# Optimization experiments

Hardware: AMD Instinct MI355X
Metric: run time of the kernel (lower is better)

The kernel has to match this reference:

```python
import jax, jax.numpy as jnp
import numpy as np

B, T, F = 1024, 512, 8        # batch, in_seq_len, n_in_feat
E, H, O, TO = 16, 32, 1, 24   # emb_size, hid_size, output_size, out_seq_len


def setup_inputs() -> dict:
    key = jax.random.key(0)
    ks = jax.random.split(key, 24)
    def n(k, shape, scale=0.1):
        return (jax.random.normal(k, shape, jnp.float32) * scale)
    return dict(
        x=jax.random.normal(ks[0], (B, T, F), jnp.float32),
        y=jax.random.normal(ks[1], (B, TO, O), jnp.float32),
        enc_emb_w=n(ks[2], (E, F)), enc_emb_b=n(ks[3], (E,)),
        enc_wih_f=n(ks[4], (3 * H, E)), enc_whh_f=n(ks[5], (3 * H, H)),
        enc_bih_f=n(ks[6], (3 * H,)), enc_bhh_f=n(ks[7], (3 * H,)),
        enc_wih_b=n(ks[8], (3 * H, E)), enc_whh_b=n(ks[9], (3 * H, H)),
        enc_bih_b=n(ks[10], (3 * H,)), enc_bhh_b=n(ks[11], (3 * H,)),
        enc_act_w=n(ks[12], (H, 2 * H)), enc_act_b=n(ks[13], (H,)),
        attn_w=n(ks[14], (H, 3 * H)),   # Linear(2H + H -> H), input order (s, enc_out)
        attn_v=n(ks[15], (1, H)),
        dec_emb_w=n(ks[16], (E, O)), dec_emb_b=n(ks[17], (E,)),
        dec_wih=n(ks[18], (3 * H, 2 * H + E)), dec_whh=n(ks[19], (3 * H, H)),
        dec_bih=n(ks[20], (3 * H,)), dec_bhh=n(ks[21], (3 * H,)),
        fc_w=n(ks[22], (O, 3 * H + E)), fc_b=n(ks[23], (O,)),
    )


def gru_cell(x_t, h, wih, whh, bih, bhh):
    # PyTorch GRU cell: gate order (r, z, n)
    gi = x_t @ wih.T + bih
    gh = h @ whh.T + bhh
    ir, iz, inn = jnp.split(gi, 3, axis=-1)
    hr, hz, hn = jnp.split(gh, 3, axis=-1)
    r = jax.nn.sigmoid(ir + hr)
    z = jax.nn.sigmoid(iz + hz)
    cand = jnp.tanh(inn + r * hn)
    return (1.0 - z) * cand + z * h


def reference(x, y, enc_emb_w, enc_emb_b, enc_wih_f, enc_whh_f, enc_bih_f, enc_bhh_f,
              enc_wih_b, enc_whh_b, enc_bih_b, enc_bhh_b, enc_act_w, enc_act_b,
              attn_w, attn_v, dec_emb_w, dec_emb_b, dec_wih, dec_whh, dec_bih, dec_bhh,
              fc_w, fc_b):
    # ----- Encoder (dropout=identity, eval mode; teacher_forcing_ratio=0 -> deterministic) -----
    xt = x.transpose(1, 0, 2)                                  # (T,B,F)
    emb = jax.nn.relu(xt @ enc_emb_w.T + enc_emb_b)            # (T,B,E)
    h0 = jnp.zeros((x.shape[0], H), x.dtype)

    def mkstep(wih, whh, bih, bhh):
        def step(h, xt_):
            hn = gru_cell(xt_, h, wih, whh, bih, bhh)
            return hn, hn
        return step

    hTf, outf = jax.lax.scan(mkstep(enc_wih_f, enc_whh_f, enc_bih_f, enc_bhh_f), h0, emb)
    hTb, outb = jax.lax.scan(mkstep(enc_wih_b, enc_whh_b, enc_bih_b, enc_bhh_b), h0, emb[::-1])
    outb = outb[::-1]
    enc_out = jnp.concatenate([outf, outb], axis=-1)            # (T,B,2H)
    s0 = jnp.tanh(jnp.concatenate([hTf, hTb], axis=-1) @ enc_act_w.T + enc_act_b)  # (B,H)

    Ws, We = attn_w[:, :H], attn_w[:, H:]                       # split concat(s, enc_out)
    enc_proj = enc_out @ We.T                                   # (T,B,H), step-invariant
    enc_out_btd = enc_out.transpose(1, 0, 2)                    # (B,T,2H)

    dec_in0 = x[:, -1, 0:1]                                     # (B,1)

    def dec_step(carry, _):
        dec_in, s = carry
        e = jnp.tanh(s @ Ws.T + enc_proj)                       # (T,B,H)
        scores = (e @ attn_v.T)[..., 0]                         # (T,B)
        # NOTE: faithful to original: torch.softmax(a, dim=1) normalizes over BATCH axis
        a = jax.nn.softmax(scores, axis=1).T                    # (B,T)
        ctx = jnp.einsum('bt,btd->bd', a, enc_out_btd)          # (B,2H)
        embd = jax.nn.relu(dec_in @ dec_emb_w.T + dec_emb_b)    # (B,E)
        rnn_in = jnp.concatenate([embd, ctx], axis=-1)          # (B,E+2H)
        s_new = gru_cell(rnn_in, s, dec_wih, dec_whh, dec_bih, dec_bhh)
        cat = jnp.concatenate([s_new, ctx, embd], axis=-1)      # (B,H+2H+E)
        pred = cat @ fc_w.T + fc_b                              # (B,O)
        return (pred, s_new), pred

    _, preds = jax.lax.scan(dec_step, (dec_in0, s0), None, length=TO)  # (TO,B,O)
    return preds.transpose(1, 0, 2)                             # (B,TO,O)
```

## Files before the change

kernel.cpp:

```cpp
#include <hip/hip_runtime.h>
#include <hip/hip_bf16.h>
#include <stdint.h>
#include <stddef.h>


#define LOG2E 1.44269504088896340736f

__device__ __forceinline__ float fast_sigmoid(float x){
    return __builtin_amdgcn_rcpf(1.f + __builtin_amdgcn_exp2f(-LOG2E * x));
}
__device__ __forceinline__ float fast_tanh(float x){
    return 1.f - 2.f * __builtin_amdgcn_rcpf(1.f + __builtin_amdgcn_exp2f(2.f * LOG2E * x));
}
__device__ __forceinline__ float bflo(unsigned u){ return __uint_as_float(u << 16); }
__device__ __forceinline__ float bfhi(unsigned u){ return __uint_as_float(u & 0xffff0000u); }
__device__ __forceinline__ float bperm(int addr, float v){
    return __int_as_float(__builtin_amdgcn_ds_bpermute(addr, __float_as_int(v)));
}

__global__ __launch_bounds__(256, 2) void enc_kernel(
    const float* __restrict__ x,
    const float* __restrict__ emb_w, const float* __restrict__ emb_b,
    const float* __restrict__ wih_f, const float* __restrict__ whh_f,
    const float* __restrict__ bih_f, const float* __restrict__ bhh_f,
    const float* __restrict__ wih_b, const float* __restrict__ whh_b,
    const float* __restrict__ bih_b, const float* __restrict__ bhh_b,
    __hip_bfloat16* __restrict__ enc_outT, float* __restrict__ hT)
{
    int tid = threadIdx.x;
    int l = tid & 63;
    int wv = tid >> 6;
    int j = l & 31;
    int p = l >> 5;
    int S = blockIdx.x * 4 + wv;
    int dir = S >> 10;
    int b = S & 1023;
    const float* wih = dir ? wih_b : wih_f;
    const float* whh = dir ? whh_b : whh_f;
    const float* bih = dir ? bih_b : bih_f;
    const float* bhh = dir ? bhh_b : bhh_f;

    float wr[8], wz[8], wn[8];
#pragma unroll
    for (int e = 0; e < 8; e++){
        int ee = 8 * p + e;
        wr[e] = wih[j * 16 + ee];
        wz[e] = wih[(32 + j) * 16 + ee];
        wn[e] = wih[(64 + j) * 16 + ee];
    }
    float ur[16], uz[16], un[16];
#pragma unroll
    for (int k = 0; k < 16; k++){
        int kk = 16 * p + k;
        ur[k] = whh[j * 32 + kk];
        uz[k] = whh[(32 + j) * 32 + kk];
        un[k] = whh[(64 + j) * 32 + kk];
    }
    float c_r  = p ? 0.f : (bih[j] + bhh[j]);
    float c_z  = p ? 0.f : (bih[32 + j] + bhh[32 + j]);
    float c_ni = p ? 0.f : bih[64 + j];
    float c_nh = p ? 0.f : bhh[64 + j];

    float ew[8];
#pragma unroll
    for (int f = 0; f < 8; f++) ew[f] = emb_w[(l & 15) * 8 + f];
    float ebias = emb_b[l & 15];

    int aE[8], aH[16];
#pragma unroll
    for (int i = 0; i < 8; i++) aE[i] = 4 * (8 * p + i);
#pragma unroll
    for (int i = 0; i < 16; i++) aH[i] = 4 * (16 * p + i);
    int aX = 4 * (l ^ 32);

    float h = 0.f;
    const float* xp = x + (size_t)b * 4096 + (dir ? 511 * 8 : 0);
    __hip_bfloat16* op = enc_outT + ((size_t)b * 512 + (dir ? 511 : 0)) * 64 + dir * 32 + j;
    int xstep = dir ? -8 : 8;
    ptrdiff_t ostep = dir ? -64 : 64;

    float4 cx0 = ((const float4*)xp)[0];
    float4 cx1 = ((const float4*)xp)[1];

    for (int it = 0; it < 512; ++it){
        const float* np = (it == 511) ? xp : (xp + xstep);
        float4 nx0 = ((const float4*)np)[0];
        float4 nx1 = ((const float4*)np)[1];

        float e0 = ebias;
        e0 = fmaf(cx0.x, ew[0], e0); e0 = fmaf(cx0.y, ew[1], e0);
        e0 = fmaf(cx0.z, ew[2], e0); e0 = fmaf(cx0.w, ew[3], e0);
        e0 = fmaf(cx1.x, ew[4], e0); e0 = fmaf(cx1.y, ew[5], e0);
        e0 = fmaf(cx1.z, ew[6], e0); e0 = fmaf(cx1.w, ew[7], e0);
        float me = fmaxf(e0, 0.f);

        float Ar = c_r, Az = c_z, Ani = c_ni, Anh = c_nh;
#pragma unroll
        for (int i = 0; i < 8; i++){
            float ev = bperm(aE[i], me);
            Ar = fmaf(ev, wr[i], Ar);
            Az = fmaf(ev, wz[i], Az);
            Ani = fmaf(ev, wn[i], Ani);
        }
#pragma unroll
        for (int i = 0; i < 16; i++){
            float hk = bperm(aH[i], h);
            Ar = fmaf(hk, ur[i], Ar);
            Az = fmaf(hk, uz[i], Az);
            Anh = fmaf(hk, un[i], Anh);
        }
        Ar  += bperm(aX, Ar);
        Az  += bperm(aX, Az);
        Ani += bperm(aX, Ani);
        Anh += bperm(aX, Anh);

        float r = fast_sigmoid(Ar);
        float z = fast_sigmoid(Az);
        float cand = fast_tanh(fmaf(r, Anh, Ani));
        h = (1.f - z) * cand + z * h;

        *op = __float2bfloat16(h);
        cx0 = nx0; cx1 = nx1;
        xp = np; op += ostep;
    }
    hT[b * 64 + dir * 32 + j] = h;
}

__global__ __launch_bounds__(256) void s0_kernel(
    const float* __restrict__ hT, const float* __restrict__ act_w, const float* __restrict__ act_b,
    const float* __restrict__ attn_w, const float* __restrict__ x,
    float* __restrict__ s, float* __restrict__ sWs, float* __restrict__ dec_in,
    float* __restrict__ denom)
{
    if (blockIdx.x == 0){
        for (int i = threadIdx.x; i < 24 * 512; i += 256) denom[i] = 0.f;
    }
    int j = threadIdx.x & 31, g = threadIdx.x >> 5;
    int b = blockIdx.x * 8 + g;
    float acc = act_b[j];
    const float4* aw = (const float4*)(act_w + j * 64);
    const float4* hp = (const float4*)(hT + b * 64);
#pragma unroll
    for (int c = 0; c < 16; c++){
        float4 wv = aw[c]; float4 hv = hp[c];
        acc = fmaf(hv.x, wv.x, acc); acc = fmaf(hv.y, wv.y, acc);
        acc = fmaf(hv.z, wv.z, acc); acc = fmaf(hv.w, wv.w, acc);
    }
    float s0v = fast_tanh(acc);
    s[b * 32 + j] = s0v;
    __shared__ float ssh[8][33];
    ssh[g][j] = s0v;
    __syncthreads();
    float a = 0.f;
    const float4* wsp = (const float4*)(attn_w + j * 96);
#pragma unroll
    for (int c = 0; c < 8; c++){
        float4 wv = wsp[c];
        a = fmaf(ssh[g][4 * c + 0], wv.x, a);
        a = fmaf(ssh[g][4 * c + 1], wv.y, a);
        a = fmaf(ssh[g][4 * c + 2], wv.z, a);
        a = fmaf(ssh[g][4 * c + 3], wv.w, a);
    }
    sWs[b * 32 + j] = a;
    if (j == 0) dec_in[b] = x[(size_t)b * 4096 + 511 * 8];
}

__global__ __launch_bounds__(256) void proj_kernel(
    const __hip_bfloat16* __restrict__ enc_outT, const float* __restrict__ attn_w,
    __hip_bfloat16* __restrict__ proj)
{
    int j = threadIdx.x & 31, g = threadIdx.x >> 5;
    float w[64];
    const float4* aw = (const float4*)(attn_w + j * 96 + 32);
#pragma unroll
    for (int c = 0; c < 16; c++){
        float4 q = aw[c];
        w[4 * c] = q.x; w[4 * c + 1] = q.y; w[4 * c + 2] = q.z; w[4 * c + 3] = q.w;
    }
    size_t base = (size_t)blockIdx.x * 256 + g * 32;
    for (int r = 0; r < 32; ++r){
        size_t pl = base + r;
        const uint4* ev = (const uint4*)(enc_outT + pl * 64);
        float acc = 0.f;
#pragma unroll
        for (int c = 0; c < 8; c++){
            uint4 pk = ev[c];
            acc = fmaf(bflo(pk.x), w[8 * c + 0], acc);
            acc = fmaf(bfhi(pk.x), w[8 * c + 1], acc);
            acc = fmaf(bflo(pk.y), w[8 * c + 2], acc);
            acc = fmaf(bfhi(pk.y), w[8 * c + 3], acc);
            acc = fmaf(bflo(pk.z), w[8 * c + 4], acc);
            acc = fmaf(bfhi(pk.z), w[8 * c + 5], acc);
            acc = fmaf(bflo(pk.w), w[8 * c + 6], acc);
            acc = fmaf(bfhi(pk.w), w[8 * c + 7], acc);
        }
        int t = (int)(pl & 511);
        int bb = (int)(pl >> 9);
        proj[((size_t)t * 1024 + bb) * 32 + j] = __float2bfloat16(acc);
    }
}

__global__ __launch_bounds__(256) void attn_kernel(
    const __hip_bfloat16* __restrict__ proj, const float* __restrict__ sWs,
    const float* __restrict__ attn_v, float* __restrict__ Ebuf, float* __restrict__ denom)
{
    int t = blockIdx.x >> 2;
    int b = (blockIdx.x & 3) * 256 + threadIdx.x;
    float v[32];
    {
        const float4* vv = (const float4*)attn_v;
#pragma unroll
        for (int c = 0; c < 8; c++){
            float4 q = vv[c];
            v[4 * c] = q.x; v[4 * c + 1] = q.y; v[4 * c + 2] = q.z; v[4 * c + 3] = q.w;
        }
    }
    const uint4* pp = (const uint4*)(proj + ((size_t)t * 1024 + b) * 32);
    const float4* sp = (const float4*)(sWs + b * 32);
    float acc = 0.f;
#pragma unroll
    for (int c = 0; c < 4; c++){
        uint4 pk = pp[c];
        float4 s0 = sp[2 * c], s1 = sp[2 * c + 1];
        acc = fmaf(v[8 * c + 0], fast_tanh(s0.x + bflo(pk.x)), acc);
        acc = fmaf(v[8 * c + 1], fast_tanh(s0.y + bfhi(pk.x)), acc);
        acc = fmaf(v[8 * c + 2], fast_tanh(s0.z + bflo(pk.y)), acc);
        acc = fmaf(v[8 * c + 3], fast_tanh(s0.w + bfhi(pk.y)), acc);
        acc = fmaf(v[8 * c + 4], fast_tanh(s1.x + bflo(pk.z)), acc);
        acc = fmaf(v[8 * c + 5], fast_tanh(s1.y + bfhi(pk.z)), acc);
        acc = fmaf(v[8 * c + 6], fast_tanh(s1.z + bflo(pk.w)), acc);
        acc = fmaf(v[8 * c + 7], fast_tanh(s1.w + bfhi(pk.w)), acc);
    }
    float Ev = __builtin_amdgcn_exp2f(LOG2E * acc);
    Ebuf[(size_t)t * 1024 + b] = Ev;
    float r = Ev;
#pragma unroll
    for (int o = 32; o >= 1; o >>= 1) r += __shfl_xor(r, o, 64);
    __shared__ float wsum[4];
    if ((threadIdx.x & 63) == 0) wsum[threadIdx.x >> 6] = r;
    __syncthreads();
    if (threadIdx.x == 0) atomicAdd(denom + t, wsum[0] + wsum[1] + wsum[2] + wsum[3]);
}

__global__ __launch_bounds__(256) void dec_kernel(
    const __hip_bfloat16* __restrict__ enc_outT, const float* __restrict__ Ebuf,
    const float* __restrict__ denom, float* __restrict__ s, float* __restrict__ sWs,
    float* __restrict__ dec_in,
    const float* __restrict__ demb_w, const float* __restrict__ demb_b,
    const float* __restrict__ dwih, const float* __restrict__ dwhh,
    const float* __restrict__ dbih, const float* __restrict__ dbhh,
    const float* __restrict__ attn_w, const float* __restrict__ fc_w,
    const float* __restrict__ fc_b, float* __restrict__ out, int step)
{
    __shared__ float w_sh[512];
    __shared__ float ctxp[4][64];
    __shared__ float rnn_sh[80];
    __shared__ float scur[32];
    __shared__ float gsum[64];
    __shared__ float gin[32], ghn[32];
    __shared__ float snew[32];
    int tid = threadIdx.x;
    int b = blockIdx.x;
    int wv = tid >> 6, l = tid & 63;

    float d0 = denom[tid], d1 = denom[tid + 256];
    float e0 = Ebuf[(size_t)tid * 1024 + b];
    float e1 = Ebuf[(size_t)(tid + 256) * 1024 + b];
    w_sh[tid] = e0 * __builtin_amdgcn_rcpf(d0);
    w_sh[tid + 256] = e1 * __builtin_amdgcn_rcpf(d1);
    if (tid < 16) rnn_sh[tid] = fmaxf(fmaf(dec_in[b], demb_w[tid], demb_b[tid]), 0.f);
    if (tid >= 32 && tid < 64) scur[tid - 32] = s[b * 32 + tid - 32];
    __syncthreads();

    float acc0 = 0.f, acc1 = 0.f, acc2 = 0.f, acc3 = 0.f;
    float acc4 = 0.f, acc5 = 0.f, acc6 = 0.f, acc7 = 0.f;
    const uint4* ep = (const uint4*)(enc_outT + (size_t)b * 32768);
#pragma unroll
    for (int i = 0; i < 16; i++){
        int idx = i * 256 + tid;
        uint4 pk = ep[idx];
        float wgt = w_sh[idx >> 3];
        acc0 = fmaf(wgt, bflo(pk.x), acc0);
        acc1 = fmaf(wgt, bfhi(pk.x), acc1);
        acc2 = fmaf(wgt, bflo(pk.y), acc2);
        acc3 = fmaf(wgt, bfhi(pk.y), acc3);
        acc4 = fmaf(wgt, bflo(pk.z), acc4);
        acc5 = fmaf(wgt, bfhi(pk.z), acc5);
        acc6 = fmaf(wgt, bflo(pk.w), acc6);
        acc7 = fmaf(wgt, bfhi(pk.w), acc7);
    }
#pragma unroll
    for (int o = 8; o <= 32; o <<= 1){
        acc0 += __shfl_xor(acc0, o, 64); acc1 += __shfl_xor(acc1, o, 64);
        acc2 += __shfl_xor(acc2, o, 64); acc3 += __shfl_xor(acc3, o, 64);
        acc4 += __shfl_xor(acc4, o, 64); acc5 += __shfl_xor(acc5, o, 64);
        acc6 += __shfl_xor(acc6, o, 64); acc7 += __shfl_xor(acc7, o, 64);
    }
    if (l < 8){
        float* cp = &ctxp[wv][l * 8];
        cp[0] = acc0; cp[1] = acc1; cp[2] = acc2; cp[3] = acc3;
        cp[4] = acc4; cp[5] = acc5; cp[6] = acc6; cp[7] = acc7;
    }
    __syncthreads();
    if (tid < 64) rnn_sh[16 + tid] = ctxp[0][tid] + ctxp[1][tid] + ctxp[2][tid] + ctxp[3][tid];
    __syncthreads();

    if (tid < 96){
        int row = tid;
        float gi = dbih[row];
        const float4* wr = (const float4*)(dwih + row * 80);
#pragma unroll
        for (int c = 0; c < 20; c++){
            float4 wv4 = wr[c];
            gi = fmaf(rnn_sh[4 * c + 0], wv4.x, gi);
            gi = fmaf(rnn_sh[4 * c + 1], wv4.y, gi);
            gi = fmaf(rnn_sh[4 * c + 2], wv4.z, gi);
            gi = fmaf(rnn_sh[4 * c + 3], wv4.w, gi);
        }
        float gh = dbhh[row];
        const float4* urow = (const float4*)(dwhh + row * 32);
#pragma unroll
        for (int c = 0; c < 8; c++){
            float4 wv4 = urow[c];
            gh = fmaf(scur[4 * c + 0], wv4.x, gh);
            gh = fmaf(scur[4 * c + 1], wv4.y, gh);
            gh = fmaf(scur[4 * c + 2], wv4.z, gh);
            gh = fmaf(scur[4 * c + 3], wv4.w, gh);
        }
        if (row < 64) gsum[row] = gi + gh;
        else { gin[row - 64] = gi; ghn[row - 64] = gh; }
    }
    __syncthreads();

    if (tid < 32){
        float r = fast_sigmoid(gsum[tid]);
        float z = fast_sigmoid(gsum[32 + tid]);
        float cand = fast_tanh(fmaf(r, ghn[tid], gin[tid]));
        float sn = (1.f - z) * cand + z * scur[tid];
        snew[tid] = sn;
        s[b * 32 + tid] = sn;
    }
    __syncthreads();

    if (tid < 32){
        float a = 0.f;
        const float4* aw = (const float4*)(attn_w + tid * 96);
#pragma unroll
        for (int c = 0; c < 8; c++){
            float4 wv4 = aw[c];
            a = fmaf(snew[4 * c + 0], wv4.x, a);
            a = fmaf(snew[4 * c + 1], wv4.y, a);
            a = fmaf(snew[4 * c + 2], wv4.z, a);
            a = fmaf(snew[4 * c + 3], wv4.w, a);
        }
        sWs[b * 32 + tid] = a;
    } else if (tid >= 64 && tid < 128){
        int ll = tid - 64;
        float cv0 = (ll < 32) ? snew[ll] : rnn_sh[ll - 16];
        float p = cv0 * fc_w[ll];
        if (ll < 48){
            int i = 64 + ll;
            float cv1 = (i < 96) ? rnn_sh[i - 16] : rnn_sh[i - 96];
            p = fmaf(cv1, fc_w[i], p);
        }
#pragma unroll
        for (int o = 32; o >= 1; o >>= 1) p += __shfl_xor(p, o, 64);
        if (ll == 0){
            float pred = p + fc_b[0];
            out[b * 24 + step] = pred;
            dec_in[b] = pred;
        }
    }
}

extern "C" void kernel_launch(void* const* d_in, const int* in_sizes, int n_in,
                              void* d_out, int out_size, void* d_ws, size_t ws_size,
                              hipStream_t stream)
{
    const float* x      = (const float*)d_in[0];
    const float* emb_w  = (const float*)d_in[2];
    const float* emb_b  = (const float*)d_in[3];
    const float* wih_f  = (const float*)d_in[4];
    const float* whh_f  = (const float*)d_in[5];
    const float* bih_f  = (const float*)d_in[6];
    const float* bhh_f  = (const float*)d_in[7];
    const float* wih_b  = (const float*)d_in[8];
    const float* whh_b  = (const float*)d_in[9];
    const float* bih_b  = (const float*)d_in[10];
    const float* bhh_b  = (const float*)d_in[11];
    const float* act_w  = (const float*)d_in[12];
    const float* act_b  = (const float*)d_in[13];
    const float* attn_w = (const float*)d_in[14];
    const float* attn_v = (const float*)d_in[15];
    const float* demb_w = (const float*)d_in[16];
    const float* demb_b = (const float*)d_in[17];
    const float* dwih   = (const float*)d_in[18];
    const float* dwhh   = (const float*)d_in[19];
    const float* dbih   = (const float*)d_in[20];
    const float* dbhh   = (const float*)d_in[21];
    const float* fc_w   = (const float*)d_in[22];
    const float* fc_b   = (const float*)d_in[23];
    (void)in_sizes; (void)n_in; (void)out_size; (void)ws_size;

    char* w = (char*)d_ws;
    __hip_bfloat16* enc_outT = (__hip_bfloat16*)w;
    __hip_bfloat16* proj     = (__hip_bfloat16*)(w + 67108864);
    float* hT     = (float*)(w + 100663296);
    float* s      = (float*)(w + 100925440);
    float* sWs    = (float*)(w + 101056512);
    float* Ebuf   = (float*)(w + 101187584);
    float* denom  = (float*)(w + 103284736);
    float* dec_in = (float*)(w + 103333888);
    float* out = (float*)d_out;

    enc_kernel<<<512, 256, 0, stream>>>(x, emb_w, emb_b, wih_f, whh_f, bih_f, bhh_f,
                                        wih_b, whh_b, bih_b, bhh_b, enc_outT, hT);
    s0_kernel<<<128, 256, 0, stream>>>(hT, act_w, act_b, attn_w, x, s, sWs, dec_in, denom);
    proj_kernel<<<2048, 256, 0, stream>>>(enc_outT, attn_w, proj);
    for (int st = 0; st < 24; ++st){
        attn_kernel<<<2048, 256, 0, stream>>>(proj, sWs, attn_v, Ebuf, denom + st * 512);
        dec_kernel<<<1024, 256, 0, stream>>>(enc_outT, Ebuf, denom + st * 512, s, sWs, dec_in,
                                             demb_w, demb_b, dwih, dwhh, dbih, dbhh,
                                             attn_w, fc_w, fc_b, out, st);
    }
}
```

Before: 1.361 ms.

## Fuse decoder loop into one persistent kernel with global grid barriers

Replaces the 48 per-step attention and decoder kernel launches with one persistent kernel of 512 blocks. The blocks loop over the 24 steps and synchronise through atomic-counter grid barriers. Each block computes one timestep's attention scores and writes that timestep's denominator directly, so no atomics into a zeroed buffer are needed. It then handles two batch rows of the context and GRU update. This removes launch overhead and inter-kernel gaps, but relies on all 512 blocks being co-resident, uses spin-waits with a timeout that could silently break correctness, and halves the parallelism of the decoder phase.

Result: slower. 4.252 ms (+212.3%).

```diff
diff --git a/kernel.cpp b/kernel.cpp
--- a/kernel.cpp
+++ b/kernel.cpp
@@ -16,6 +16,21 @@
 __device__ __forceinline__ float bfhi(unsigned u){ return __uint_as_float(u & 0xffff0000u); }
 __device__ __forceinline__ float bperm(int addr, float v){
     return __int_as_float(__builtin_amdgcn_ds_bpermute(addr, __float_as_int(v)));
+}
+
+__device__ __forceinline__ void gbar(unsigned* ctr, unsigned target){
+    __syncthreads();
+    if (threadIdx.x == 0){
+        __threadfence();
+        atomicAdd(ctr, 1u);
+        unsigned spins = 0;
+        while (atomicAdd(ctr, 0u) < target && spins < 2000000u){
+            __builtin_amdgcn_s_sleep(8);
+            ++spins;
+        }
+        __threadfence();
+    }
+    __syncthreads();
 }
 
 __global__ __launch_bounds__(256, 2) void enc_kernel(
@@ -130,11 +145,9 @@
     const float* __restrict__ hT, const float* __restrict__ act_w, const float* __restrict__ act_b,
     const float* __restrict__ attn_w, const float* __restrict__ x,
     float* __restrict__ s, float* __restrict__ sWs, float* __restrict__ dec_in,
-    float* __restrict__ denom)
+    unsigned* __restrict__ bar)
 {
-    if (blockIdx.x == 0){
-        for (int i = threadIdx.x; i < 24 * 512; i += 256) denom[i] = 0.f;
-    }
+    if (blockIdx.x == 0 && threadIdx.x < 64) bar[threadIdx.x] = 0u;
     int j = threadIdx.x & 31, g = threadIdx.x >> 5;
     int b = blockIdx.x * 8 + g;
     float acc = act_b[j];
@@ -200,176 +213,177 @@
     }
 }
 
-__global__ __launch_bounds__(256) void attn_kernel(
-    const __hip_bfloat16* __restrict__ proj, const float* __restrict__ sWs,
-    const float* __restrict__ attn_v, float* __restrict__ Ebuf, float* __restrict__ denom)
-{
-    int t = blockIdx.x >> 2;
-    int b = (blockIdx.x & 3) * 256 + threadIdx.x;
-    float v[32];
-    {
-        const float4* vv = (const float4*)attn_v;
-#pragma unroll
-        for (int c = 0; c < 8; c++){
-            float4 q = vv[c];
-            v[4 * c] = q.x; v[4 * c + 1] = q.y; v[4 * c + 2] = q.z; v[4 * c + 3] = q.w;
-        }
-    }
-    const uint4* pp = (const uint4*)(proj + ((size_t)t * 1024 + b) * 32);
-    const float4* sp = (const float4*)(sWs + b * 32);
-    float acc = 0.f;
-#pragma unroll
-    for (int c = 0; c < 4; c++){
-        uint4 pk = pp[c];
-        float4 s0 = sp[2 * c], s1 = sp[2 * c + 1];
-        acc = fmaf(v[8 * c + 0], fast_tanh(s0.x + bflo(pk.x)), acc);
-        acc = fmaf(v[8 * c + 1], fast_tanh(s0.y + bfhi(pk.x)), acc);
-        acc = fmaf(v[8 * c + 2], fast_tanh(s0.z + bflo(pk.y)), acc);
-        acc = fmaf(v[8 * c + 3], fast_tanh(s0.w + bfhi(pk.y)), acc);
-        acc = fmaf(v[8 * c + 4], fast_tanh(s1.x + bflo(pk.z)), acc);
-        acc = fmaf(v[8 * c + 5], fast_tanh(s1.y + bfhi(pk.z)), acc);
-        acc = fmaf(v[8 * c + 6], fast_tanh(s1.z + bflo(pk.w)), acc);
-        acc = fmaf(v[8 * c + 7], fast_tanh(s1.w + bfhi(pk.w)), acc);
-    }
-    float Ev = __builtin_amdgcn_exp2f(LOG2E * acc);
-    Ebuf[(size_t)t * 1024 + b] = Ev;
-    float r = Ev;
-#pragma unroll
-    for (int o = 32; o >= 1; o >>= 1) r += __shfl_xor(r, o, 64);
-    __shared__ float wsum[4];
-    if ((threadIdx.x & 63) == 0) wsum[threadIdx.x >> 6] = r;
-    __syncthreads();
-    if (threadIdx.x == 0) atomicAdd(denom + t, wsum[0] + wsum[1] + wsum[2] + wsum[3]);
-}
-
-__global__ __launch_bounds__(256) void dec_kernel(
-    const __hip_bfloat16* __restrict__ enc_outT, const float* __restrict__ Ebuf,
-    const float* __restrict__ denom, float* __restrict__ s, float* __restrict__ sWs,
-    float* __restrict__ dec_in,
+__global__ __launch_bounds__(256, 2) void dec_fused(
+    const __hip_bfloat16* __restrict__ enc_outT, const __hip_bfloat16* __restrict__ proj,
+    float* __restrict__ Ebuf, float* __restrict__ denom,
+    float* __restrict__ s, float* __restrict__ sWs, float* __restrict__ dec_in,
     const float* __restrict__ demb_w, const float* __restrict__ demb_b,
     const float* __restrict__ dwih, const float* __restrict__ dwhh,
     const float* __restrict__ dbih, const float* __restrict__ dbhh,
-    const float* __restrict__ attn_w, const float* __restrict__ fc_w,
-    const float* __restrict__ fc_b, float* __restrict__ out, int step)
+    const float* __restrict__ attn_w, const float* __restrict__ attn_v,
+    const float* __restrict__ fc_w, const float* __restrict__ fc_b,
+    float* __restrict__ out, unsigned* __restrict__ bar)
 {
+    int tid = threadIdx.x;
+    int g = blockIdx.x;
+    int wv = tid >> 6, l = tid & 63;
+
     __shared__ float w_sh[512];
+    __shared__ float redsh[4];
     __shared__ float ctxp[4][64];
     __shared__ float rnn_sh[80];
     __shared__ float scur[32];
     __shared__ float gsum[64];
     __shared__ float gin[32], ghn[32];
     __shared__ float snew[32];
-    int tid = threadIdx.x;
-    int b = blockIdx.x;
-    int wv = tid >> 6, l = tid & 63;
-
-    float d0 = denom[tid], d1 = denom[tid + 256];
-    float e0 = Ebuf[(size_t)tid * 1024 + b];
-    float e1 = Ebuf[(size_t)(tid + 256) * 1024 + b];
-    w_sh[tid] = e0 * __builtin_amdgcn_rcpf(d0);
-    w_sh[tid + 256] = e1 * __builtin_amdgcn_rcpf(d1);
-    if (tid < 16) rnn_sh[tid] = fmaxf(fmaf(dec_in[b], demb_w[tid], demb_b[tid]), 0.f);
-    if (tid >= 32 && tid < 64) scur[tid - 32] = s[b * 32 + tid - 32];
-    __syncthreads();
-
-    float acc0 = 0.f, acc1 = 0.f, acc2 = 0.f, acc3 = 0.f;
-    float acc4 = 0.f, acc5 = 0.f, acc6 = 0.f, acc7 = 0.f;
-    const uint4* ep = (const uint4*)(enc_outT + (size_t)b * 32768);
-#pragma unroll
-    for (int i = 0; i < 16; i++){
-        int idx = i * 256 + tid;
-        uint4 pk = ep[idx];
-        float wgt = w_sh[idx >> 3];
-        acc0 = fmaf(wgt, bflo(pk.x), acc0);
-        acc1 = fmaf(wgt, bfhi(pk.x), acc1);
-        acc2 = fmaf(wgt, bflo(pk.y), acc2);
-        acc3 = fmaf(wgt, bfhi(pk.y), acc3);
-        acc4 = fmaf(wgt, bflo(pk.z), acc4);
-        acc5 = fmaf(wgt, bfhi(pk.z), acc5);
-        acc6 = fmaf(wgt, bflo(pk.w), acc6);
-        acc7 = fmaf(wgt, bfhi(pk.w), acc7);
-    }
-#pragma unroll
-    for (int o = 8; o <= 32; o <<= 1){
-        acc0 += __shfl_xor(acc0, o, 64); acc1 += __shfl_xor(acc1, o, 64);
-        acc2 += __shfl_xor(acc2, o, 64); acc3 += __shfl_xor(acc3, o, 64);
-        acc4 += __shfl_xor(acc4, o, 64); acc5 += __shfl_xor(acc5, o, 64);
-        acc6 += __shfl_xor(acc6, o, 64); acc7 += __shfl_xor(acc7, o, 64);
-    }
-    if (l < 8){
-        float* cp = &ctxp[wv][l * 8];
-        cp[0] = acc0; cp[1] = acc1; cp[2] = acc2; cp[3] = acc3;
-        cp[4] = acc4; cp[5] = acc5; cp[6] = acc6; cp[7] = acc7;
-    }
-    __syncthreads();
-    if (tid < 64) rnn_sh[16 + tid] = ctxp[0][tid] + ctxp[1][tid] + ctxp[2][tid] + ctxp[3][tid];
-    __syncthreads();
-
-    if (tid < 96){
-        int row = tid;
-        float gi = dbih[row];
-        const float4* wr = (const float4*)(dwih + row * 80);
-#pragma unroll
-        for (int c = 0; c < 20; c++){
-            float4 wv4 = wr[c];
-            gi = fmaf(rnn_sh[4 * c + 0], wv4.x, gi);
-            gi = fmaf(rnn_sh[4 * c + 1], wv4.y, gi);
-            gi = fmaf(rnn_sh[4 * c + 2], wv4.z, gi);
-            gi = fmaf(rnn_sh[4 * c + 3], wv4.w, gi);
-        }
-        float gh = dbhh[row];
-        const float4* urow = (const float4*)(dwhh + row * 32);
-#pragma unroll
-        for (int c = 0; c < 8; c++){
-            float4 wv4 = urow[c];
-            gh = fmaf(scur[4 * c + 0], wv4.x, gh);
-            gh = fmaf(scur[4 * c + 1], wv4.y, gh);
-            gh = fmaf(scur[4 * c + 2], wv4.z, gh);
-            gh = fmaf(scur[4 * c + 3], wv4.w, gh);
-        }
-        if (row < 64) gsum[row] = gi + gh;
-        else { gin[row - 64] = gi; ghn[row - 64] = gh; }
-    }
-    __syncthreads();
-
-    if (tid < 32){
-        float r = fast_sigmoid(gsum[tid]);
-        float z = fast_sigmoid(gsum[32 + tid]);
-        float cand = fast_tanh(fmaf(r, ghn[tid], gin[tid]));
-        float sn = (1.f - z) * cand + z * scur[tid];
-        snew[tid] = sn;
-        s[b * 32 + tid] = sn;
-    }
-    __syncthreads();
-
-    if (tid < 32){
-        float a = 0.f;
-        const float4* aw = (const float4*)(attn_w + tid * 96);
-#pragma unroll
-        for (int c = 0; c < 8; c++){
-            float4 wv4 = aw[c];
-            a = fmaf(snew[4 * c + 0], wv4.x, a);
-            a = fmaf(snew[4 * c + 1], wv4.y, a);
-            a = fmaf(snew[4 * c + 2], wv4.z, a);
-            a = fmaf(snew[4 * c + 3], wv4.w, a);
-        }
-        sWs[b * 32 + tid] = a;
-    } else if (tid >= 64 && tid < 128){
-        int ll = tid - 64;
-        float cv0 = (ll < 32) ? snew[ll] : rnn_sh[ll - 16];
-        float p = cv0 * fc_w[ll];
-        if (ll < 48){
-            int i = 64 + ll;
-            float cv1 = (i < 96) ? rnn_sh[i - 16] : rnn_sh[i - 96];
-            p = fmaf(cv1, fc_w[i], p);
-        }
-#pragma unroll
-        for (int o = 32; o >= 1; o >>= 1) p += __shfl_xor(p, o, 64);
-        if (ll == 0){
-            float pred = p + fc_b[0];
-            out[b * 24 + step] = pred;
-            dec_in[b] = pred;
-        }
+
+    for (int st = 0; st < 24; ++st){
+        {
+            int t = g;
+            float part = 0.f;
+#pragma unroll
+            for (int half = 0; half < 4; ++half){
+                int b = half * 256 + tid;
+                const uint4* pp = (const uint4*)(proj + ((size_t)t * 1024 + b) * 32);
+                const float4* sp = (const float4*)(sWs + b * 32);
+                float acc = 0.f;
+#pragma unroll
+                for (int c = 0; c < 4; c++){
+                    uint4 pk = pp[c];
+                    float4 s0 = sp[2 * c], s1 = sp[2 * c + 1];
+                    acc = fmaf(attn_v[8 * c + 0], fast_tanh(s0.x + bflo(pk.x)), acc);
+                    acc = fmaf(attn_v[8 * c + 1], fast_tanh(s0.y + bfhi(pk.x)), acc);
+                    acc = fmaf(attn_v[8 * c + 2], fast_tanh(s0.z + bflo(pk.y)), acc);
+                    acc = fmaf(attn_v[8 * c + 3], fast_tanh(s0.w + bfhi(pk.y)), acc);
+                    acc = fmaf(attn_v[8 * c + 4], fast_tanh(s1.x + bflo(pk.z)), acc);
+                    acc = fmaf(attn_v[8 * c + 5], fast_tanh(s1.y + bfhi(pk.z)), acc);
+                    acc = fmaf(attn_v[8 * c + 6], fast_tanh(s1.z + bflo(pk.w)), acc);
+                    acc = fmaf(attn_v[8 * c + 7], fast_tanh(s1.w + bfhi(pk.w)), acc);
+                }
+                float Ev = __builtin_amdgcn_exp2f(LOG2E * acc);
+                Ebuf[(size_t)t * 1024 + b] = Ev;
+                part += Ev;
+            }
+#pragma unroll
+            for (int o = 32; o >= 1; o >>= 1) part += __shfl_xor(part, o, 64);
+            if (l == 0) redsh[wv] = part;
+            __syncthreads();
+            if (tid == 0) denom[t] = redsh[0] + redsh[1] + redsh[2] + redsh[3];
+        }
+        gbar(bar + 2 * st, 512);
+
+        float inv0 = __builtin_amdgcn_rcpf(denom[tid]);
+        float inv1 = __builtin_amdgcn_rcpf(denom[tid + 256]);
+        for (int bb = 0; bb < 2; ++bb){
+            int b = g + bb * 512;
+            __syncthreads();
+            w_sh[tid] = Ebuf[(size_t)tid * 1024 + b] * inv0;
+            w_sh[tid + 256] = Ebuf[(size_t)(tid + 256) * 1024 + b] * inv1;
+            if (tid < 16) rnn_sh[tid] = fmaxf(fmaf(dec_in[b], demb_w[tid], demb_b[tid]), 0.f);
+            if (tid >= 32 && tid < 64) scur[tid - 32] = s[b * 32 + tid - 32];
+            __syncthreads();
+
+            float acc0 = 0.f, acc1 = 0.f, acc2 = 0.f, acc3 = 0.f;
+            float acc4 = 0.f, acc5 = 0.f, acc6 = 0.f, acc7 = 0.f;
+            const uint4* ep = (const uint4*)(enc_outT + (size_t)b * 32768);
+#pragma unroll
+            for (int i = 0; i < 16; i++){
+                int idx = i * 256 + tid;
+                uint4 pk = ep[idx];
+                float wgt = w_sh[idx >> 3];
+                acc0 = fmaf(wgt, bflo(pk.x), acc0);
+                acc1 = fmaf(wgt, bfhi(pk.x), acc1);
+                acc2 = fmaf(wgt, bflo(pk.y), acc2);
+                acc3 = fmaf(wgt, bfhi(pk.y), acc3);
+                acc4 = fmaf(wgt, bflo(pk.z), acc4);
+                acc5 = fmaf(wgt, bfhi(pk.z), acc5);
+                acc6 = fmaf(wgt, bflo(pk.w), acc6);
+                acc7 = fmaf(wgt, bfhi(pk.w), acc7);
+            }
+#pragma unroll
+            for (int o = 8; o <= 32; o <<= 1){
+                acc0 += __shfl_xor(acc0, o, 64); acc1 += __shfl_xor(acc1, o, 64);
+                acc2 += __shfl_xor(acc2, o, 64); acc3 += __shfl_xor(acc3, o, 64);
+                acc4 += __shfl_xor(acc4, o, 64); acc5 += __shfl_xor(acc5, o, 64);
+                acc6 += __shfl_xor(acc6, o, 64); acc7 += __shfl_xor(acc7, o, 64);
+            }
+            if (l < 8){
+                float* cp = &ctxp[wv][l * 8];
+                cp[0] = acc0; cp[1] = acc1; cp[2] = acc2; cp[3] = acc3;
+                cp[4] = acc4; cp[5] = acc5; cp[6] = acc6; cp[7] = acc7;
+            }
+            __syncthreads();
+            if (tid < 64) rnn_sh[16 + tid] = ctxp[0][tid] + ctxp[1][tid] + ctxp[2][tid] + ctxp[3][tid];
+            __syncthreads();
+
+            if (tid < 96){
+                int row = tid;
+                float gi = dbih[row];
+                const float4* wr = (const float4*)(dwih + row * 80);
+#pragma unroll
+                for (int c = 0; c < 20; c++){
+                    float4 wv4 = wr[c];
+                    gi = fmaf(rnn_sh[4 * c + 0], wv4.x, gi);
+                    gi = fmaf(rnn_sh[4 * c + 1], wv4.y, gi);
+                    gi = fmaf(rnn_sh[4 * c + 2], wv4.z, gi);
+                    gi = fmaf(rnn_sh[4 * c + 3], wv4.w, gi);
+                }
+                float gh = dbhh[row];
+                const float4* urow = (const float4*)(dwhh + row * 32);
+#pragma unroll
+                for (int c = 0; c < 8; c++){
+                    float4 wv4 = urow[c];
+                    gh = fmaf(scur[4 * c + 0], wv4.x, gh);
+                    gh = fmaf(scur[4 * c + 1], wv4.y, gh);
+                    gh = fmaf(scur[4 * c + 2], wv4.z, gh);
+                    gh = fmaf(scur[4 * c + 3], wv4.w, gh);
+                }
+                if (row < 64) gsum[row] = gi + gh;
+                else { gin[row - 64] = gi; ghn[row - 64] = gh; }
+            }
+            __syncthreads();
+
+            if (tid < 32){
+                float r = fast_sigmoid(gsum[tid]);
+                float z = fast_sigmoid(gsum[32 + tid]);
+                float cand = fast_tanh(fmaf(r, ghn[tid], gin[tid]));
+                float sn = (1.f - z) * cand + z * scur[tid];
+                snew[tid] = sn;
+                s[b * 32 + tid] = sn;
+            }
+            __syncthreads();
+
+            if (tid < 32){
+                float a = 0.f;
+                const float4* aw = (const float4*)(attn_w + tid * 96);
+#pragma unroll
+                for (int c = 0; c < 8; c++){
+                    float4 wv4 = aw[c];
+                    a = fmaf(snew[4 * c + 0], wv4.x, a);
+                    a = fmaf(snew[4 * c + 1], wv4.y, a);
+                    a = fmaf(snew[4 * c + 2], wv4.z, a);
+                    a = fmaf(snew[4 * c + 3], wv4.w, a);
+                }
+                sWs[b * 32 + tid] = a;
+            } else if (tid >= 64 && tid < 128){
+                int ll = tid - 64;
+                float cv0 = (ll < 32) ? snew[ll] : rnn_sh[ll - 16];
+                float p = cv0 * fc_w[ll];
+                if (ll < 48){
+                    int i = 64 + ll;
+                    float cv1 = (i < 96) ? rnn_sh[i - 16] : rnn_sh[i - 96];
+                    p = fmaf(cv1, fc_w[i], p);
+                }
+#pragma unroll
+                for (int o = 32; o >= 1; o >>= 1) p += __shfl_xor(p, o, 64);
+                if (ll == 0){
+                    float pred = p + fc_b[0];
+                    out[b * 24 + st] = pred;
+                    dec_in[b] = pred;
+                }
+            }
+        }
+        gbar(bar + 2 * st + 1, 512);
     }
 }
 
@@ -410,17 +424,15 @@
     float* sWs    = (float*)(w + 101056512);
     float* Ebuf   = (float*)(w + 101187584);
     float* denom  = (float*)(w + 103284736);
+    unsigned* bar = (unsigned*)(w + 103286784);
     float* dec_in = (float*)(w + 103333888);
     float* out = (float*)d_out;
 
     enc_kernel<<<512, 256, 0, stream>>>(x, emb_w, emb_b, wih_f, whh_f, bih_f, bhh_f,
                                         wih_b, whh_b, bih_b, bhh_b, enc_outT, hT);
-    s0_kernel<<<128, 256, 0, stream>>>(hT, act_w, act_b, attn_w, x, s, sWs, dec_in, denom);
+    s0_kernel<<<128, 256, 0, stream>>>(hT, act_w, act_b, attn_w, x, s, sWs, dec_in, bar);
     proj_kernel<<<2048, 256, 0, stream>>>(enc_outT, attn_w, proj);
-    for (int st = 0; st < 24; ++st){
-        attn_kernel<<<2048, 256, 0, stream>>>(proj, sWs, attn_v, Ebuf, denom + st * 512);
-        dec_kernel<<<1024, 256, 0, stream>>>(enc_outT, Ebuf, denom + st * 512, s, sWs, dec_in,
-                                             demb_w, demb_b, dwih, dwhh, dbih, dbhh,
-                                             attn_w, fc_w, fc_b, out, st);
-    }
-}
+    dec_fused<<<512, 256, 0, stream>>>(enc_outT, proj, Ebuf, denom, s, sWs, dec_in,
+                                       demb_w, demb_b, dwih, dwhh, dbih, dbhh,
+                                       attn_w, attn_v, fc_w, fc_b, out, bar);
+}
```
